# Performance work log

Hardware: AMD Instinct MI355X
Metric: run time of the kernel (lower is better)

The kernel has to match this reference:

```python
import jax, jax.numpy as jnp
import numpy as np

# graph sizes
G, P, EP = 128, 256, 1024          # graphs, nodes/graph, edges/graph
N, E = G * P, G * EP
C, KENS, S = 4, 2, 1               # centroids, ensembles, samples
R = S * KENS                       # repeats
F, DE, D, OUT = 64, 16, 128, 10


def setup_inputs() -> dict:
    key = jax.random.key(0)
    ks = jax.random.split(key, 24)
    off = (jnp.arange(G, dtype=jnp.int32) * P)[:, None]
    src = (jax.random.randint(ks[0], (G, EP), 0, P, dtype=jnp.int32) + off).reshape(-1)
    dst = (jax.random.randint(ks[1], (G, EP), 0, P, dtype=jnp.int32) + off).reshape(-1)
    edge_index = jnp.stack([src, dst])            # [2, E], edges stay within graphs
    batch = jnp.repeat(jnp.arange(G, dtype=jnp.int32), P)  # [N]
    rn = lambda k, shp, s: jax.random.normal(k, shp, jnp.float32) * s
    return {
        "x_feat": rn(ks[2], (N, F), 1.0),
        "edge_attr": rn(ks[3], (E, DE), 1.0),
        "W_atom": rn(ks[4], (F, D), 0.1), "b_atom": jnp.zeros((D,), jnp.float32),
        "W_score": rn(ks[5], (D, C * KENS), 0.1),
        "W_edge": rn(ks[6], (DE, D), 0.1),
        "W_b2c": rn(ks[7], (D, D), 0.1),
        "W_bb": rn(ks[8], (D, D), 0.1), "W_bc": rn(ks[9], (D, D), 0.1),
        "W_cb": rn(ks[10], (D, D), 0.1), "W_cc": rn(ks[11], (D, D), 0.1),
        "W_sb": rn(ks[12], (D, D), 0.1), "W_sc": rn(ks[13], (D, D), 0.1),
        "W_inter": rn(ks[14], (D, D), 0.1), "b_inter": jnp.zeros((D,), jnp.float32),
        "W_out": rn(ks[15], (D, OUT), 0.1), "b_out": jnp.zeros((OUT,), jnp.float32),
        "edge_index": edge_index, "batch": batch,
    }


def reference(x_feat, edge_attr, W_atom, b_atom, W_score, W_edge, W_b2c,
              W_bb, W_bc, W_cb, W_cc, W_sb, W_sc, W_inter, b_inter,
              W_out, b_out, edge_index, batch):
    src, dst = edge_index[0], edge_index[1]
    # atom encoder + scorer + softmax sampler (marginals)
    x = x_feat @ W_atom + b_atom                                  # [N,D]
    scores = (x @ W_score).reshape(N, C, KENS)
    marg = jax.nn.softmax(scores, axis=1)                         # over centroids
    nm = jnp.broadcast_to(marg[None], (S, N, C, KENS))            # [S,N,C,KENS]
    nm = jnp.transpose(nm, (0, 3, 2, 1)).reshape(R, C, N)         # [R,C,N]
    em = nm[:, :, src] * nm[:, :, dst]                            # edge_mask [R,C,E]
    # base2centroid: masked MP on base graph + weighted segment-mean pooling
    edge_emb = edge_attr @ W_edge                                 # [E,D]
    h = jax.nn.relu(x @ W_b2c)                                    # [N,D]
    m = h[src] + edge_emb                                         # [E,D]
    agg = jnp.zeros((R, C, N, D), m.dtype).at[:, :, dst].add(em[..., None] * m)
    hm = h[None, None] + agg                                      # [R,C,N,D]
    denom = jnp.zeros((R, C, G), nm.dtype).at[:, :, batch].add(nm)
    num = jnp.zeros((R, C, G, D), hm.dtype).at[:, :, batch].add(nm[..., None] * hm)
    cent_x = jnp.transpose(num / (denom[..., None] + 1e-6), (0, 2, 1, 3))  # [R,G,C,D]
    # intra centroid-pair edge weights: triu pairs + diag, scatter over graphs
    iu, ju = np.triu_indices(C, 1)
    pi = np.concatenate([iu, np.arange(C)])
    pj = np.concatenate([ju, np.arange(C)])
    e2g = batch[src]
    w = jnp.zeros((R, pi.size, G), nm.dtype).at[:, :, e2g].add(
        nm[:, pi][:, :, src] * nm[:, pj][:, :, dst])              # [R,10,G]
    w = w.at[:, -C:, :].multiply(0.5)                             # halve diagonal counts
    wt = jnp.transpose(w, (0, 2, 1))                              # [R,G,10]
    Wcc = jnp.zeros((R, G, C, C), nm.dtype)
    Wcc = Wcc.at[:, :, pi, pj].add(wt).at[:, :, pj, pi].add(wt)   # to_undirected
    dg = jnp.arange(C)
    Wcc = Wcc.at[:, :, dg, dg].multiply(0.5)                      # self loops counted once
    Wcc = Wcc / (jax.lax.stop_gradient(jnp.max(Wcc)) + 1e-9)      # detached-max norm
    # hetero GNN layer: base->base, base->centroid, centroid->centroid, centroid->base
    agg_bb = jnp.zeros((N, D), x.dtype).at[dst].add(x[src] + edge_emb)           # [N,D]
    agg_bc = jnp.transpose(
        jnp.zeros((R, C, G, D), x.dtype).at[:, :, batch].add(nm[..., None] * x[None, None]),
        (0, 2, 1, 3))                                             # [R,G,C,D]
    agg_cc = jnp.einsum('rgij,rgjd->rgid', Wcc, cent_x)
    h_cent = jax.nn.relu(agg_bc @ W_bc + agg_cc @ W_cc + cent_x @ W_sc)          # [R,G,C,D]
    agg_cb = jnp.einsum('rcn,rncd->rnd', nm, h_cent[:, batch])                   # [R,N,D]
    h_base = jax.nn.relu(agg_bb[None] @ W_bb + agg_cb @ W_cb + x[None] @ W_sb)   # [R,N,D]
    # inter-ensemble mean pool, inter head, intra mean graph pool, intra head
    node_emb = jnp.mean(h_base, axis=0) @ W_inter + b_inter                      # [N,D]
    graph_emb = jnp.zeros((G, D), node_emb.dtype).at[batch].add(node_emb) / P    # [G,D]
    return graph_emb @ W_out + b_out                                             # [G,OUT]
```

## Files before the change

kernel.cpp:

```cpp
#include <hip/hip_runtime.h>
#include <hip/hip_bf16.h>

#define Nn 32768
#define Ee 131072
#define Gg 128
#define Dd 128
#define ASTR 1032

using bf16 = __hip_bfloat16;
typedef __attribute__((ext_vector_type(8))) short bf16x8;
typedef __attribute__((ext_vector_type(4))) float f32x4;

__device__ __forceinline__ float b2f(bf16 v){ return __bfloat162float(v); }
__device__ __forceinline__ bf16  f2b(float v){ return __float2bfloat16(v); }
__device__ __forceinline__ unsigned short bf16bits(float v){
  union { bf16 b; unsigned short u; } cv; cv.b = f2b(v); return cv.u;
}
__device__ __forceinline__ unsigned int packxh(float xv, float hv){
  return ((unsigned int)bf16bits(hv) << 16) | (unsigned int)bf16bits(xv);
}
__device__ __forceinline__ float upk_x(unsigned int v){ return __uint_as_float(v << 16); }
__device__ __forceinline__ float upk_h(unsigned int v){ return __uint_as_float(v & 0xffff0000u); }

__global__ __launch_bounds__(128)
void k_wrep(const float* __restrict__ Wbb, const float* __restrict__ Wsb,
            const float* __restrict__ Wcb, unsigned short* __restrict__ Wbbp,
            unsigned short* __restrict__ Wsbp, unsigned short* __restrict__ Wcbp) {
  int mat = blockIdx.x >> 7, n = blockIdx.x & 127, k = threadIdx.x;
  const float* src = (mat == 0) ? Wbb : (mat == 1) ? Wsb : Wcb;
  unsigned short* dst = (mat == 0) ? Wbbp : (mat == 1) ? Wsbp : Wcbp;
  dst[n*128 + k] = bf16bits(src[k*128 + n]);
}

__global__ __launch_bounds__(256)
void k_atom(const float* __restrict__ xf, const float* __restrict__ Wa,
            const float* __restrict__ ba, const float* __restrict__ Wsc,
            const float* __restrict__ Wb2c,
            unsigned int* __restrict__ xh, float* __restrict__ nmt) {
  __shared__ float sxf[32*64];
  __shared__ float sx[32*128];
  __shared__ float ss[32*8];
  __shared__ float sWsc[1024];
  int tid = threadIdx.x, n0 = blockIdx.x * 32;
  int ct = tid & 31, rt = tid >> 5;
  int c0 = ct*4, r0 = rt*4;
  for (int j = tid; j < 2048; j += 256) sxf[j] = xf[n0*64 + j];
  for (int j = tid; j < 1024; j += 256) sWsc[j] = Wsc[j];
  __syncthreads();
  float acc[4][4];
  #pragma unroll
  for (int i = 0; i < 4; ++i)
    #pragma unroll
    for (int j = 0; j < 4; ++j) acc[i][j] = ba[c0+j];
  for (int k = 0; k < 64; ++k) {
    float4 bv = *reinterpret_cast<const float4*>(&Wa[k*128 + c0]);
    #pragma unroll
    for (int i = 0; i < 4; ++i) {
      float a = sxf[(r0+i)*64 + k];
      acc[i][0] += a*bv.x; acc[i][1] += a*bv.y; acc[i][2] += a*bv.z; acc[i][3] += a*bv.w;
    }
  }
  #pragma unroll
  for (int i = 0; i < 4; ++i)
    #pragma unroll
    for (int j = 0; j < 4; ++j) sx[(r0+i)*128 + c0+j] = acc[i][j];
  __syncthreads();
  {
    int node = tid >> 3, col = tid & 7;
    float s = 0.f;
    for (int d = 0; d < 128; ++d) s += sx[node*128 + d] * sWsc[d*8 + col];
    ss[node*8 + col] = s;
  }
  __syncthreads();
  if (tid < 64) {
    int node = tid >> 1, k = tid & 1;
    float v0 = ss[node*8 + 0 + k], v1 = ss[node*8 + 2 + k];
    float v2 = ss[node*8 + 4 + k], v3 = ss[node*8 + 6 + k];
    float mx = fmaxf(fmaxf(v0, v1), fmaxf(v2, v3));
    float e0 = expf(v0-mx), e1 = expf(v1-mx), e2 = expf(v2-mx), e3 = expf(v3-mx);
    float inv = 1.f / (e0+e1+e2+e3);
    size_t nb = (size_t)(n0 + node)*8 + k*4;
    nmt[nb+0] = e0*inv; nmt[nb+1] = e1*inv; nmt[nb+2] = e2*inv; nmt[nb+3] = e3*inv;
  }
  float acc2[4][4];
  #pragma unroll
  for (int i = 0; i < 4; ++i)
    #pragma unroll
    for (int j = 0; j < 4; ++j) acc2[i][j] = 0.f;
  for (int k = 0; k < 128; ++k) {
    float4 bv = *reinterpret_cast<const float4*>(&Wb2c[k*128 + c0]);
    #pragma unroll
    for (int i = 0; i < 4; ++i) {
      float a = sx[(r0+i)*128 + k];
      acc2[i][0] += a*bv.x; acc2[i][1] += a*bv.y; acc2[i][2] += a*bv.z; acc2[i][3] += a*bv.w;
    }
  }
  #pragma unroll
  for (int i = 0; i < 4; ++i)
    #pragma unroll
    for (int j = 0; j < 4; ++j)
      xh[(size_t)(n0+r0+i)*128 + c0+j] = packxh(acc[i][j], fmaxf(acc2[i][j], 0.f));
}

__global__ __launch_bounds__(256)
void k_csr(const int* __restrict__ ei, const float* __restrict__ nmt,
           const float* __restrict__ ea,
           int* __restrict__ osrc, int* __restrict__ rowstart,
           float* __restrict__ sea, float* __restrict__ den) {
  __shared__ int cnt[256], off[256], sdl[1024], sorder[1024];
  __shared__ float sden[256*8];
  int t = threadIdx.x, g = blockIdx.x;
  cnt[t] = 0;
  __syncthreads();
  #pragma unroll
  for (int j = 0; j < 4; ++j) {
    int e = t + j*256;
    int dl = ei[Ee + g*1024 + e] - g*256;
    sdl[e] = dl;
    atomicAdd(&cnt[dl], 1);
  }
  {
    const float4* p = reinterpret_cast<const float4*>(nmt + (size_t)(g*256 + t)*8);
    float4 a = p[0], b = p[1];
    sden[t*8+0]=a.x; sden[t*8+1]=a.y; sden[t*8+2]=a.z; sden[t*8+3]=a.w;
    sden[t*8+4]=b.x; sden[t*8+5]=b.y; sden[t*8+6]=b.z; sden[t*8+7]=b.w;
  }
  __syncthreads();
  off[t] = cnt[t];
  __syncthreads();
  for (int s = 1; s < 256; s <<= 1) {
    int v = (t >= s) ? off[t - s] : 0;
    __syncthreads();
    off[t] += v;
    __syncthreads();
  }
  int startv = off[t] - cnt[t];
  int mycnt = cnt[t];
  rowstart[g*256 + t] = startv;
  off[t] = startv;
  __syncthreads();
  #pragma unroll
  for (int j = 0; j < 4; ++j) {
    int e = t + j*256;
    int pos = atomicAdd(&off[sdl[e]], 1);
    sorder[pos] = e;
    osrc[g*1024 + pos] = ei[g*1024 + e];
  }
  __syncthreads();
  float s0x=0,s0y=0,s0z=0,s0w=0, s1x=0,s1y=0,s1z=0,s1w=0;
  float s2x=0,s2y=0,s2z=0,s2w=0, s3x=0,s3y=0,s3z=0,s3w=0;
  for (int jj = startv; jj < startv + mycnt; ++jj) {
    int e = sorder[jj];
    const float4* er = reinterpret_cast<const float4*>(ea + ((size_t)g*1024 + e)*16);
    float4 a0 = er[0], a1 = er[1], a2 = er[2], a3 = er[3];
    s0x+=a0.x; s0y+=a0.y; s0z+=a0.z; s0w+=a0.w;
    s1x+=a1.x; s1y+=a1.y; s1z+=a1.z; s1w+=a1.w;
    s2x+=a2.x; s2y+=a2.y; s2z+=a2.z; s2w+=a2.w;
    s3x+=a3.x; s3y+=a3.y; s3z+=a3.z; s3w+=a3.w;
  }
  float4* so = reinterpret_cast<float4*>(sea + (size_t)(g*256 + t)*16);
  so[0] = make_float4(s0x,s0y,s0z,s0w);
  so[1] = make_float4(s1x,s1y,s1z,s1w);
  so[2] = make_float4(s2x,s2y,s2z,s2w);
  so[3] = make_float4(s3x,s3y,s3z,s3w);
  if (t < 8) {
    float s = 0.f;
    for (int p = 0; p < 256; ++p) s += sden[p*8 + t];
    den[t*Gg + g] = s;
  }
}

__global__ __launch_bounds__(256)
void k_edgesc(const int* __restrict__ ei, const float* __restrict__ nmt,
              const float* __restrict__ ea, float* __restrict__ wcc,
              unsigned int* __restrict__ maxbits, float* __restrict__ bnm,
              float* __restrict__ gea) {
  __shared__ float salpha[8*ASTR];
  __shared__ float sbeta[8*256];
  __shared__ float red[20];
  __shared__ float geap[4*128];
  int t = threadIdx.x, g = blockIdx.x;
  for (int j = t; j < 2048; j += 256) sbeta[j] = 0.f;
  if (t < 20) red[t] = 0.f;
  __syncthreads();
  float w[20];
  #pragma unroll
  for (int i = 0; i < 20; ++i) w[i] = 0.f;
  #pragma unroll
  for (int j = 0; j < 4; ++j) {
    int e = t + j*256;
    int s = ei[g*1024 + e], dd = ei[Ee + g*1024 + e];
    const float4* ps4 = reinterpret_cast<const float4*>(nmt + (size_t)s*8);
    const float4* pt4 = reinterpret_cast<const float4*>(nmt + (size_t)dd*8);
    float4 sv0 = ps4[0], sv1 = ps4[1], tv0 = pt4[0], tv1 = pt4[1];
    float ps[8] = {sv0.x,sv0.y,sv0.z,sv0.w,sv1.x,sv1.y,sv1.z,sv1.w};
    float pt[8] = {tv0.x,tv0.y,tv0.z,tv0.w,tv1.x,tv1.y,tv1.z,tv1.w};
    #pragma unroll
    for (int r = 0; r < 2; ++r) {
      int b = r*4;
      w[r*10+0] += ps[b+0]*pt[b+1]; w[r*10+1] += ps[b+0]*pt[b+2]; w[r*10+2] += ps[b+0]*pt[b+3];
      w[r*10+3] += ps[b+1]*pt[b+2]; w[r*10+4] += ps[b+1]*pt[b+3]; w[r*10+5] += ps[b+2]*pt[b+3];
      w[r*10+6] += ps[b+0]*pt[b+0]; w[r*10+7] += ps[b+1]*pt[b+1];
      w[r*10+8] += ps[b+2]*pt[b+2]; w[r*10+9] += ps[b+3]*pt[b+3];
    }
    int sl = s - g*256;
    #pragma unroll
    for (int rc = 0; rc < 8; ++rc) {
      float al = ps[rc]*pt[rc]*pt[rc];
      salpha[rc*ASTR + e] = al;
      atomicAdd(&sbeta[rc*256 + sl], al);
    }
  }
  #pragma unroll
  for (int i = 0; i < 20; ++i) {
    for (int off2 = 32; off2 > 0; off2 >>= 1) w[i] += __shfl_down(w[i], off2);
  }
  if ((t & 63) == 0) {
    #pragma unroll
    for (int i = 0; i < 20; ++i) atomicAdd(&red[i], w[i]);
  }
  __syncthreads();
  if (t < 32) {
    int r = t >> 4, ij = t & 15, i = ij >> 2, j = ij & 3;
    float v;
    if (i == j) v = 0.5f * red[r*10 + 6 + i];
    else { int a = i < j ? i : j, b = i < j ? j : i;
           int p = (a == 0) ? (b - 1) : (a == 1) ? (b + 1) : 5;
           v = red[r*10 + p]; }
    wcc[(r*Gg + g)*16 + ij] = v;
    atomicMax(maxbits, __float_as_uint(v));
  }
  int wv = t >> 6, l = t & 63;
  int j16 = l & 15, rb = l >> 4;
  float acc0 = 0.f, acc1 = 0.f;
  int ebase = wv*256;
  for (int ee = 0; ee < 256; ++ee) {
    float eav = ea[((size_t)g*1024 + ebase + ee)*16 + j16];
    acc0 += salpha[rb*ASTR + ebase + ee] * eav;
    acc1 += salpha[(rb+4)*ASTR + ebase + ee] * eav;
  }
  geap[wv*128 + l]      = acc0;
  geap[wv*128 + 64 + l] = acc1;
  __syncthreads();
  if (t < 128) {
    float s = geap[t] + geap[128+t] + geap[256+t] + geap[384+t];
    int rc = t >> 4, j = t & 15;
    gea[((size_t)rc*Gg + g)*16 + j] = s;
  }
  {
    float b0 = sbeta[0*256+t], b1 = sbeta[1*256+t], b2 = sbeta[2*256+t], b3 = sbeta[3*256+t];
    float b4 = sbeta[4*256+t], b5 = sbeta[5*256+t], b6 = sbeta[6*256+t], b7 = sbeta[7*256+t];
    float4* bo = reinterpret_cast<float4*>(bnm + (size_t)(g*256 + t)*8);
    bo[0] = make_float4(b0,b1,b2,b3);
    bo[1] = make_float4(b4,b5,b6,b7);
  }
}

__global__ __launch_bounds__(256)
void k_gather(const unsigned int* __restrict__ xh, const float* __restrict__ nmt,
              const float* __restrict__ bnm, const float* __restrict__ sea,
              const float* __restrict__ We, const int* __restrict__ osrc,
              const int* __restrict__ rowstart,
              unsigned short* __restrict__ aggbb16, float* __restrict__ pnum,
              float* __restrict__ pabc) {
  __shared__ float combN[8*128], combA[8*128];
  int t = threadIdx.x, d = t & 127, q = t >> 7;
  int g = blockIdx.x >> 4, e16 = blockIdx.x & 15;
  int nbase = g*256 + e16*16;
  float w[16];
  #pragma unroll
  for (int j = 0; j < 16; ++j) w[j] = We[j*128 + d];
  float aH[8] = {0,0,0,0,0,0,0,0};
  float aX[8] = {0,0,0,0,0,0,0,0};
  for (int nn = q; nn < 16; nn += 2) {
    int n = nbase + nn;
    unsigned int vn = xh[(size_t)n*128 + d];
    float xn = upk_x(vn), hn = upk_h(vn);
    const float4* pp = reinterpret_cast<const float4*>(nmt + (size_t)n*8);
    float4 p0 = pp[0], p1 = pp[1];
    float pc[8] = {p0.x,p0.y,p0.z,p0.w,p1.x,p1.y,p1.z,p1.w};
    const float4* bp = reinterpret_cast<const float4*>(bnm + (size_t)n*8);
    float4 b0 = bp[0], b1 = bp[1];
    float bt[8] = {b0.x,b0.y,b0.z,b0.w,b1.x,b1.y,b1.z,b1.w};
    #pragma unroll
    for (int rc = 0; rc < 8; ++rc) {
      aH[rc] += (pc[rc] + bt[rc])*hn;
      aX[rc] += pc[rc]*xn;
    }
    const float4* sp = reinterpret_cast<const float4*>(sea + (size_t)n*16);
    float4 s0 = sp[0], s1 = sp[1], s2 = sp[2], s3 = sp[3];
    float agg = s0.x*w[0] + s0.y*w[1] + s0.z*w[2] + s0.w*w[3]
              + s1.x*w[4] + s1.y*w[5] + s1.z*w[6] + s1.w*w[7]
              + s2.x*w[8] + s2.y*w[9] + s2.z*w[10]+ s2.w*w[11]
              + s3.x*w[12]+ s3.y*w[13]+ s3.z*w[14]+ s3.w*w[15];
    int ln = n - g*256;
    int start = rowstart[n];
    int end = (ln == 255) ? 1024 : rowstart[n+1];
    for (int jj = start; jj < end; ++jj) {
      int sg = osrc[g*1024 + jj];
      agg += upk_x(xh[(size_t)sg*128 + d]);
    }
    aggbb16[(size_t)n*128 + d] = bf16bits(agg);
  }
  if (q == 1) {
    #pragma unroll
    for (int rc = 0; rc < 8; ++rc) { combN[rc*128+d] = aH[rc]; combA[rc*128+d] = aX[rc]; }
  }
  __syncthreads();
  if (q == 0) {
    #pragma unroll
    for (int rc = 0; rc < 8; ++rc) {
      pnum[(((size_t)rc*Gg + g)*16 + e16)*128 + d] = aH[rc] + combN[rc*128+d];
      pabc[(((size_t)rc*Gg + g)*16 + e16)*128 + d] = aX[rc] + combA[rc*128+d];
    }
  }
}

__global__ __launch_bounds__(128)
void k_hcent(const float* __restrict__ pnum, const float* __restrict__ den,
             const float* __restrict__ pabc, const float* __restrict__ gea,
             const float* __restrict__ We, const float* __restrict__ wcc,
             const unsigned int* __restrict__ maxbits,
             const float* __restrict__ Wbc, const float* __restrict__ Wcc_,
             const float* __restrict__ Wsc2, float* __restrict__ hcent) {
  __shared__ float scent[512], sbc[512], sccs[512], swcc[16];
  int tid = threadIdx.x, r = blockIdx.x >> 7, g = blockIdx.x & 127;
  float inv = 1.f / (__uint_as_float(*maxbits) + 1e-9f);
  if (tid < 16) swcc[tid] = wcc[(r*Gg + g)*16 + tid] * inv;
  for (int c = 0; c < 4; ++c) {
    int rc = r*4 + c;
    float nv = 0.f, av = 0.f;
    #pragma unroll
    for (int s = 0; s < 16; ++s) {
      nv += pnum[(((size_t)rc*Gg + g)*16 + s)*128 + tid];
      av += pabc[(((size_t)rc*Gg + g)*16 + s)*128 + tid];
    }
    const float* geag = gea + ((size_t)rc*Gg + g)*16;
    #pragma unroll
    for (int j = 0; j < 16; ++j) nv += geag[j] * We[j*128 + tid];
    float dn = den[rc*Gg + g] + 1e-6f;
    scent[c*128 + tid] = nv / dn;
    sbc[c*128 + tid]   = av;
  }
  __syncthreads();
  for (int i = 0; i < 4; ++i) {
    sccs[i*128 + tid] = swcc[i*4+0]*scent[tid]       + swcc[i*4+1]*scent[128 + tid]
                      + swcc[i*4+2]*scent[256 + tid] + swcc[i*4+3]*scent[384 + tid];
  }
  __syncthreads();
  float acc[4] = {0.f, 0.f, 0.f, 0.f};
  for (int k = 0; k < 128; ++k) {
    float wb = Wbc[k*128 + tid], wc = Wcc_[k*128 + tid], ws2 = Wsc2[k*128 + tid];
    #pragma unroll
    for (int c = 0; c < 4; ++c)
      acc[c] += sbc[c*128 + k]*wb + sccs[c*128 + k]*wc + scent[c*128 + k]*ws2;
  }
  #pragma unroll
  for (int c = 0; c < 4; ++c)
    hcent[((r*Gg + g)*4 + c)*128 + tid] = fmaxf(acc[c], 0.f);
}

__global__ __launch_bounds__(256)
void k_hbase(const unsigned short* __restrict__ aggbb16,
             const unsigned int* __restrict__ xh,
             const float* __restrict__ nmt, const float* __restrict__ hcent,
             const unsigned short* __restrict__ Wbbp,
             const unsigned short* __restrict__ Wsbp,
             const unsigned short* __restrict__ Wcbp,
             float* __restrict__ gsum) {
  __shared__ unsigned short A1[64*136];
  __shared__ unsigned short A2[64*136];
  __shared__ float shc[512];
  __shared__ float snm[256];
  __shared__ float pred[128];
  int tid = threadIdx.x, n0 = blockIdx.x*64, g = n0 >> 8;
  int lane = tid & 63, wv = tid >> 6;
  int m = lane & 15, quad = lane >> 4;
  int rbase = wv*16;
  for (int j = tid; j < 1024; j += 256) {
    int row = j >> 4, col = (j & 15) * 8;
    uint4 v = *reinterpret_cast<const uint4*>(aggbb16 + (size_t)(n0+row)*128 + col);
    *reinterpret_cast<uint4*>(&A1[row*136 + col]) = v;
  }
  for (int j = tid; j < 2048; j += 256) {
    int row = j >> 5, col = (j & 31) * 4;
    uint4 v = *reinterpret_cast<const uint4*>(xh + (size_t)(n0+row)*128 + col);
    uint2 o;
    o.x = (v.x & 0xffffu) | (v.y << 16);
    o.y = (v.z & 0xffffu) | (v.w << 16);
    *reinterpret_cast<uint2*>(&A2[row*136 + col]) = o;
  }
  __syncthreads();
  f32x4 bb[8];
  #pragma unroll
  for (int nt = 0; nt < 8; ++nt) bb[nt] = (f32x4){0.f,0.f,0.f,0.f};
  const short* a1r = (const short*)&A1[(rbase + m)*136];
  const short* a2r = (const short*)&A2[(rbase + m)*136];
  #pragma unroll
  for (int nt = 0; nt < 8; ++nt) {
    #pragma unroll
    for (int kk = 0; kk < 4; ++kk) {
      int ko = kk*32 + quad*8;
      bf16x8 av1 = *reinterpret_cast<const bf16x8*>(a1r + ko);
      bf16x8 wv1 = *reinterpret_cast<const bf16x8*>((const short*)Wbbp + (nt*16 + m)*128 + ko);
      bb[nt] = __builtin_amdgcn_mfma_f32_16x16x32_bf16(av1, wv1, bb[nt], 0, 0, 0);
      bf16x8 av2 = *reinterpret_cast<const bf16x8*>(a2r + ko);
      bf16x8 wv2 = *reinterpret_cast<const bf16x8*>((const short*)Wsbp + (nt*16 + m)*128 + ko);
      bb[nt] = __builtin_amdgcn_mfma_f32_16x16x32_bf16(av2, wv2, bb[nt], 0, 0, 0);
    }
  }
  __syncthreads();
  unsigned short* SB = A2;
  f32x4 msum[8];
  #pragma unroll
  for (int nt = 0; nt < 8; ++nt) msum[nt] = (f32x4){0.f,0.f,0.f,0.f};
  for (int r = 0; r < 2; ++r) {
    for (int j = tid; j < 512; j += 256) shc[j] = hcent[((size_t)(r*Gg + g)*4)*128 + j];
    if (tid < 256) snm[tid] = nmt[(size_t)(n0 + (tid >> 2))*8 + r*4 + (tid & 3)];
    __syncthreads();
    for (int j = tid; j < 8192; j += 256) {
      int node = j >> 7, k = j & 127;
      float v = snm[node*4+0]*shc[k]       + snm[node*4+1]*shc[128 + k]
              + snm[node*4+2]*shc[256 + k] + snm[node*4+3]*shc[384 + k];
      SB[node*136 + k] = bf16bits(v);
    }
    __syncthreads();
    f32x4 aw[8];
    #pragma unroll
    for (int nt = 0; nt < 8; ++nt) aw[nt] = (f32x4){0.f,0.f,0.f,0.f};
    const short* sbr = (const short*)&SB[(rbase + m)*136];
    #pragma unroll
    for (int nt = 0; nt < 8; ++nt) {
      #pragma unroll
      for (int kk = 0; kk < 4; ++kk) {
        int ko = kk*32 + quad*8;
        bf16x8 av = *reinterpret_cast<const bf16x8*>(sbr + ko);
        bf16x8 wvv = *reinterpret_cast<const bf16x8*>((const short*)Wcbp + (nt*16 + m)*128 + ko);
        aw[nt] = __builtin_amdgcn_mfma_f32_16x16x32_bf16(av, wvv, aw[nt], 0, 0, 0);
      }
    }
    #pragma unroll
    for (int nt = 0; nt < 8; ++nt) {
      #pragma unroll
      for (int i = 0; i < 4; ++i)
        msum[nt][i] += 0.5f * fmaxf(bb[nt][i] + aw[nt][i], 0.f);
    }
    __syncthreads();
  }
  if (tid < 128) pred[tid] = 0.f;
  __syncthreads();
  #pragma unroll
  for (int nt = 0; nt < 8; ++nt) {
    float s = msum[nt][0] + msum[nt][1] + msum[nt][2] + msum[nt][3];
    atomicAdd(&pred[nt*16 + m], s);
  }
  __syncthreads();
  if (tid < 128) atomicAdd(&gsum[g*128 + tid], pred[tid]);
}

__global__ __launch_bounds__(128)
void k_out(const float* __restrict__ gsum, const float* __restrict__ Wint,
           const float* __restrict__ bint, const float* __restrict__ Wout,
           const float* __restrict__ bout, float* __restrict__ out) {
  __shared__ float ss[128], sge[128];
  int tid = threadIdx.x, g = blockIdx.x;
  ss[tid] = gsum[g*128 + tid] * (1.f/256.f);
  __syncthreads();
  float ge = bint[tid];
  for (int k = 0; k < 128; ++k) ge += ss[k] * Wint[k*128 + tid];
  sge[tid] = ge;
  __syncthreads();
  if (tid < 10) {
    float o = bout[tid];
    for (int d = 0; d < 128; ++d) o += sge[d] * Wout[d*10 + tid];
    out[g*10 + tid] = o;
  }
}

extern "C" void kernel_launch(void* const* d_in, const int* in_sizes, int n_in,
                              void* d_out, int out_size, void* d_ws, size_t ws_size,
                              hipStream_t stream) {
  const float* xf   = (const float*)d_in[0];
  const float* ea   = (const float*)d_in[1];
  const float* Wa   = (const float*)d_in[2];
  const float* ba   = (const float*)d_in[3];
  const float* Wsc  = (const float*)d_in[4];
  const float* We   = (const float*)d_in[5];
  const float* Wb2c = (const float*)d_in[6];
  const float* Wbb  = (const float*)d_in[7];
  const float* Wbc  = (const float*)d_in[8];
  const float* Wcb  = (const float*)d_in[9];
  const float* WccW = (const float*)d_in[10];
  const float* Wsb  = (const float*)d_in[11];
  const float* Wsc2 = (const float*)d_in[12];
  const float* Wint = (const float*)d_in[13];
  const float* bint = (const float*)d_in[14];
  const float* Wout = (const float*)d_in[15];
  const float* bout = (const float*)d_in[16];
  const int*   ei   = (const int*)d_in[17];

  float* ws    = (float*)d_ws;
  unsigned int* xh = (unsigned int*)ws;
  float* nmt   = ws + 4194304;
  float* hcent = ws + 4456448;
  float* wcc   = ws + 4587520;
  unsigned short* aggbb16 = (unsigned short*)(ws + 4591616);
  int*   osrc  = (int*)(ws + 6688768);
  int*   rowst = (int*)(ws + 6819840);
  float* sea   = ws + 6852608;
  float* bnm   = ws + 7376896;
  float* gea   = ws + 7639040;
  float* pnum  = ws + 7655424;
  float* pabc  = ws + 9752576;
  float* den   = ws + 11849728;
  float* gsum  = ws + 11850752;
  unsigned int* maxbits = (unsigned int*)(ws + 11867136);
  unsigned short* Wbbp = (unsigned short*)(ws + 11867200);
  unsigned short* Wsbp = (unsigned short*)(ws + 11875392);
  unsigned short* Wcbp = (unsigned short*)(ws + 11883584);

  hipMemsetAsync(gsum, 0, (16384 + 64) * sizeof(float), stream);

  k_wrep  <<<3*128, 128, 0, stream>>>(Wbb, Wsb, Wcb, Wbbp, Wsbp, Wcbp);
  k_atom  <<<Nn/32, 256, 0, stream>>>(xf, Wa, ba, Wsc, Wb2c, xh, nmt);
  k_csr   <<<Gg,    256, 0, stream>>>(ei, nmt, ea, osrc, rowst, sea, den);
  k_edgesc<<<Gg,    256, 0, stream>>>(ei, nmt, ea, wcc, maxbits, bnm, gea);
  k_gather<<<Gg*16, 256, 0, stream>>>(xh, nmt, bnm, sea, We, osrc, rowst,
                                      aggbb16, pnum, pabc);
  k_hcent <<<2*Gg,  128, 0, stream>>>(pnum, den, pabc, gea, We, wcc, maxbits,
                                      Wbc, WccW, Wsc2, hcent);
  k_hbase <<<Nn/64, 256, 0, stream>>>(aggbb16, xh, nmt, hcent, Wbbp, Wsbp, Wcbp, gsum);
  k_out   <<<Gg,    128, 0, stream>>>(gsum, Wint, bint, Wout, bout, (float*)d_out);
}
```

Baseline: 293.3 us.

## Use MFMA for atom encoder, fuse CSR and edge-score kernels, split gather

The atom encoder and b2c projection move from scalar fp32 FMA loops to bf16 MFMA 16x16x32, with transposed bf16 copies of W_atom and W_b2c prepared in the weight-repack kernel. The CSR build and the edge-scoring kernel are merged into one per-graph kernel that stages edge attributes in LDS chunks and accumulates per-node edge-attr sums with shared atomics. The old gather kernel is split into a pooling kernel and an edge-aggregation kernel with finer granularity, giving more blocks. The aim is to cut scalar compute and kernel-launch and global-read overhead. The cost is bf16 rounding of the x activations before the score and b2c products, plus heavier LDS atomic traffic.

```diff
diff --git a/kernel.cpp b/kernel.cpp
--- a/kernel.cpp
+++ b/kernel.cpp
@@ -5,7 +5,6 @@
 #define Ee 131072
 #define Gg 128
 #define Dd 128
-#define ASTR 1032
 
 using bf16 = __hip_bfloat16;
 typedef __attribute__((ext_vector_type(8))) short bf16x8;
@@ -16,114 +15,160 @@
 __device__ __forceinline__ unsigned short bf16bits(float v){
   union { bf16 b; unsigned short u; } cv; cv.b = f2b(v); return cv.u;
 }
-__device__ __forceinline__ unsigned int packxh(float xv, float hv){
-  return ((unsigned int)bf16bits(hv) << 16) | (unsigned int)bf16bits(xv);
+__device__ __forceinline__ float bfu(unsigned short u){
+  return __uint_as_float((unsigned int)u << 16);
 }
 __device__ __forceinline__ float upk_x(unsigned int v){ return __uint_as_float(v << 16); }
 __device__ __forceinline__ float upk_h(unsigned int v){ return __uint_as_float(v & 0xffff0000u); }
 
 __global__ __launch_bounds__(128)
 void k_wrep(const float* __restrict__ Wbb, const float* __restrict__ Wsb,
-            const float* __restrict__ Wcb, unsigned short* __restrict__ Wbbp,
-            unsigned short* __restrict__ Wsbp, unsigned short* __restrict__ Wcbp) {
+            const float* __restrict__ Wcb, const float* __restrict__ Wa,
+            const float* __restrict__ Wb2c,
+            unsigned short* __restrict__ Wbbp, unsigned short* __restrict__ Wsbp,
+            unsigned short* __restrict__ Wcbp, unsigned short* __restrict__ Wap,
+            unsigned short* __restrict__ Wb2cp) {
   int mat = blockIdx.x >> 7, n = blockIdx.x & 127, k = threadIdx.x;
-  const float* src = (mat == 0) ? Wbb : (mat == 1) ? Wsb : Wcb;
-  unsigned short* dst = (mat == 0) ? Wbbp : (mat == 1) ? Wsbp : Wcbp;
-  dst[n*128 + k] = bf16bits(src[k*128 + n]);
+  if      (mat == 0) Wbbp [n*128 + k] = bf16bits(Wbb [k*128 + n]);
+  else if (mat == 1) Wsbp [n*128 + k] = bf16bits(Wsb [k*128 + n]);
+  else if (mat == 2) Wcbp [n*128 + k] = bf16bits(Wcb [k*128 + n]);
+  else if (mat == 3) { if (k < 64) Wap[n*64 + k] = bf16bits(Wa[k*128 + n]); }
+  else               Wb2cp[n*128 + k] = bf16bits(Wb2c[k*128 + n]);
 }
 
 __global__ __launch_bounds__(256)
-void k_atom(const float* __restrict__ xf, const float* __restrict__ Wa,
+void k_atom(const float* __restrict__ xf, const unsigned short* __restrict__ Wap,
             const float* __restrict__ ba, const float* __restrict__ Wsc,
-            const float* __restrict__ Wb2c,
+            const unsigned short* __restrict__ Wb2cp,
             unsigned int* __restrict__ xh, float* __restrict__ nmt) {
-  __shared__ float sxf[32*64];
-  __shared__ float sx[32*128];
-  __shared__ float ss[32*8];
+  __shared__ unsigned short sxf[64*72];
+  __shared__ unsigned short sxb[64*136];
+  __shared__ float ss[64*8];
   __shared__ float sWsc[1024];
-  int tid = threadIdx.x, n0 = blockIdx.x * 32;
-  int ct = tid & 31, rt = tid >> 5;
-  int c0 = ct*4, r0 = rt*4;
-  for (int j = tid; j < 2048; j += 256) sxf[j] = xf[n0*64 + j];
+  int tid = threadIdx.x, n0 = blockIdx.x*64;
+  int lane = tid & 63, wv = tid >> 6;
+  int m = lane & 15, quad = lane >> 4;
+  int rbase = wv*16;
+  #pragma unroll
+  for (int k = 0; k < 4; ++k) {
+    int pos = (tid + k*256)*4;
+    int node = pos >> 6, f = pos & 63;
+    float4 v = *reinterpret_cast<const float4*>(xf + (size_t)n0*64 + pos);
+    ushort4 o;
+    o.x = bf16bits(v.x); o.y = bf16bits(v.y); o.z = bf16bits(v.z); o.w = bf16bits(v.w);
+    *reinterpret_cast<ushort4*>(&sxf[node*72 + f]) = o;
+  }
   for (int j = tid; j < 1024; j += 256) sWsc[j] = Wsc[j];
   __syncthreads();
-  float acc[4][4];
-  #pragma unroll
-  for (int i = 0; i < 4; ++i)
-    #pragma unroll
-    for (int j = 0; j < 4; ++j) acc[i][j] = ba[c0+j];
-  for (int k = 0; k < 64; ++k) {
-    float4 bv = *reinterpret_cast<const float4*>(&Wa[k*128 + c0]);
-    #pragma unroll
-    for (int i = 0; i < 4; ++i) {
-      float a = sxf[(r0+i)*64 + k];
-      acc[i][0] += a*bv.x; acc[i][1] += a*bv.y; acc[i][2] += a*bv.z; acc[i][3] += a*bv.w;
-    }
-  }
-  #pragma unroll
-  for (int i = 0; i < 4; ++i)
-    #pragma unroll
-    for (int j = 0; j < 4; ++j) sx[(r0+i)*128 + c0+j] = acc[i][j];
-  __syncthreads();
-  {
-    int node = tid >> 3, col = tid & 7;
+  f32x4 cx[8];
+  #pragma unroll
+  for (int nt = 0; nt < 8; ++nt) {
+    float bv = ba[nt*16 + m];
+    cx[nt] = (f32x4){bv, bv, bv, bv};
+  }
+  const unsigned short* a1 = &sxf[(rbase + m)*72];
+  #pragma unroll
+  for (int nt = 0; nt < 8; ++nt) {
+    #pragma unroll
+    for (int kk = 0; kk < 2; ++kk) {
+      int ko = kk*32 + quad*8;
+      bf16x8 av = *reinterpret_cast<const bf16x8*>((const short*)a1 + ko);
+      bf16x8 bv8 = *reinterpret_cast<const bf16x8*>((const short*)Wap + (nt*16 + m)*64 + ko);
+      cx[nt] = __builtin_amdgcn_mfma_f32_16x16x32_bf16(av, bv8, cx[nt], 0, 0, 0);
+    }
+  }
+  #pragma unroll
+  for (int nt = 0; nt < 8; ++nt)
+    #pragma unroll
+    for (int i = 0; i < 4; ++i)
+      sxb[(rbase + quad*4 + i)*136 + nt*16 + m] = bf16bits(cx[nt][i]);
+  __syncthreads();
+  for (int p = tid; p < 512; p += 256) {
+    int node = p >> 3, col = p & 7;
     float s = 0.f;
-    for (int d = 0; d < 128; ++d) s += sx[node*128 + d] * sWsc[d*8 + col];
+    for (int dd = 0; dd < 128; ++dd)
+      s += bfu(sxb[node*136 + dd]) * sWsc[dd*8 + col];
     ss[node*8 + col] = s;
   }
   __syncthreads();
-  if (tid < 64) {
+  if (tid < 128) {
     int node = tid >> 1, k = tid & 1;
     float v0 = ss[node*8 + 0 + k], v1 = ss[node*8 + 2 + k];
     float v2 = ss[node*8 + 4 + k], v3 = ss[node*8 + 6 + k];
     float mx = fmaxf(fmaxf(v0, v1), fmaxf(v2, v3));
     float e0 = expf(v0-mx), e1 = expf(v1-mx), e2 = expf(v2-mx), e3 = expf(v3-mx);
     float inv = 1.f / (e0+e1+e2+e3);
-    size_t nb = (size_t)(n0 + node)*8 + k*4;
-    nmt[nb+0] = e0*inv; nmt[nb+1] = e1*inv; nmt[nb+2] = e2*inv; nmt[nb+3] = e3*inv;
-  }
-  float acc2[4][4];
-  #pragma unroll
-  for (int i = 0; i < 4; ++i)
-    #pragma unroll
-    for (int j = 0; j < 4; ++j) acc2[i][j] = 0.f;
-  for (int k = 0; k < 128; ++k) {
-    float4 bv = *reinterpret_cast<const float4*>(&Wb2c[k*128 + c0]);
+    *reinterpret_cast<float4*>(nmt + (size_t)(n0 + node)*8 + k*4) =
+        make_float4(e0*inv, e1*inv, e2*inv, e3*inv);
+  }
+  f32x4 chf[8];
+  #pragma unroll
+  for (int nt = 0; nt < 8; ++nt) chf[nt] = (f32x4){0.f,0.f,0.f,0.f};
+  const unsigned short* a2 = &sxb[(rbase + m)*136];
+  #pragma unroll
+  for (int nt = 0; nt < 8; ++nt) {
+    #pragma unroll
+    for (int kk = 0; kk < 4; ++kk) {
+      int ko = kk*32 + quad*8;
+      bf16x8 av = *reinterpret_cast<const bf16x8*>((const short*)a2 + ko);
+      bf16x8 bv8 = *reinterpret_cast<const bf16x8*>((const short*)Wb2cp + (nt*16 + m)*128 + ko);
+      chf[nt] = __builtin_amdgcn_mfma_f32_16x16x32_bf16(av, bv8, chf[nt], 0, 0, 0);
+    }
+  }
+  #pragma unroll
+  for (int nt = 0; nt < 8; ++nt) {
     #pragma unroll
     for (int i = 0; i < 4; ++i) {
-      float a = sx[(r0+i)*128 + k];
-      acc2[i][0] += a*bv.x; acc2[i][1] += a*bv.y; acc2[i][2] += a*bv.z; acc2[i][3] += a*bv.w;
-    }
-  }
-  #pragma unroll
-  for (int i = 0; i < 4; ++i)
-    #pragma unroll
-    for (int j = 0; j < 4; ++j)
-      xh[(size_t)(n0+r0+i)*128 + c0+j] = packxh(acc[i][j], fmaxf(acc2[i][j], 0.f));
+      int row = rbase + quad*4 + i, col = nt*16 + m;
+      float hv = fmaxf(chf[nt][i], 0.f);
+      unsigned short xb = sxb[row*136 + col];
+      xh[(size_t)(n0 + row)*128 + col] =
+          ((unsigned int)bf16bits(hv) << 16) | (unsigned int)xb;
+    }
+  }
 }
 
 __global__ __launch_bounds__(256)
-void k_csr(const int* __restrict__ ei, const float* __restrict__ nmt,
-           const float* __restrict__ ea,
-           int* __restrict__ osrc, int* __restrict__ rowstart,
-           float* __restrict__ sea, float* __restrict__ den) {
-  __shared__ int cnt[256], off[256], sdl[1024], sorder[1024];
-  __shared__ float sden[256*8];
+void k_graph(const int* __restrict__ ei, const float* __restrict__ nmt,
+             const float* __restrict__ ea,
+             int* __restrict__ osrc, int* __restrict__ rowstart,
+             float* __restrict__ sea, float* __restrict__ den,
+             float* __restrict__ wcc, unsigned int* __restrict__ maxbits,
+             float* __restrict__ bnm, float* __restrict__ gea) {
+  __shared__ int sdl[1024], ssl[1024];
+  __shared__ int cnt[256], off[256];
+  __shared__ float eabuf[256*16];
+  __shared__ float salpha[8*258];
+  __shared__ float sbeta[8*256];
+  __shared__ float seaacc[256*17];
+  __shared__ float red[20];
+  __shared__ float sga[256];
+  __shared__ float den8[8];
   int t = threadIdx.x, g = blockIdx.x;
   cnt[t] = 0;
+  for (int j = t; j < 2048; j += 256) sbeta[j] = 0.f;
+  for (int j = t; j < 4352; j += 256) seaacc[j] = 0.f;
+  if (t < 20) red[t] = 0.f;
+  if (t < 8) den8[t] = 0.f;
   __syncthreads();
   #pragma unroll
   for (int j = 0; j < 4; ++j) {
     int e = t + j*256;
+    int sl = ei[g*1024 + e] - g*256;
     int dl = ei[Ee + g*1024 + e] - g*256;
-    sdl[e] = dl;
+    ssl[e] = sl; sdl[e] = dl;
     atomicAdd(&cnt[dl], 1);
   }
   {
     const float4* p = reinterpret_cast<const float4*>(nmt + (size_t)(g*256 + t)*8);
     float4 a = p[0], b = p[1];
-    sden[t*8+0]=a.x; sden[t*8+1]=a.y; sden[t*8+2]=a.z; sden[t*8+3]=a.w;
-    sden[t*8+4]=b.x; sden[t*8+5]=b.y; sden[t*8+6]=b.z; sden[t*8+7]=b.w;
+    float v[8] = {a.x,a.y,a.z,a.w,b.x,b.y,b.z,b.w};
+    #pragma unroll
+    for (int i = 0; i < 8; ++i) {
+      float s = v[i];
+      for (int o = 32; o > 0; o >>= 1) s += __shfl_xor(s, o);
+      if ((t & 63) == 0) atomicAdd(&den8[i], s);
+    }
   }
   __syncthreads();
   off[t] = cnt[t];
@@ -135,7 +180,6 @@
     __syncthreads();
   }
   int startv = off[t] - cnt[t];
-  int mycnt = cnt[t];
   rowstart[g*256 + t] = startv;
   off[t] = startv;
   __syncthreads();
@@ -143,82 +187,67 @@
   for (int j = 0; j < 4; ++j) {
     int e = t + j*256;
     int pos = atomicAdd(&off[sdl[e]], 1);
-    sorder[pos] = e;
-    osrc[g*1024 + pos] = ei[g*1024 + e];
-  }
-  __syncthreads();
-  float s0x=0,s0y=0,s0z=0,s0w=0, s1x=0,s1y=0,s1z=0,s1w=0;
-  float s2x=0,s2y=0,s2z=0,s2w=0, s3x=0,s3y=0,s3z=0,s3w=0;
-  for (int jj = startv; jj < startv + mycnt; ++jj) {
-    int e = sorder[jj];
-    const float4* er = reinterpret_cast<const float4*>(ea + ((size_t)g*1024 + e)*16);
-    float4 a0 = er[0], a1 = er[1], a2 = er[2], a3 = er[3];
-    s0x+=a0.x; s0y+=a0.y; s0z+=a0.z; s0w+=a0.w;
-    s1x+=a1.x; s1y+=a1.y; s1z+=a1.z; s1w+=a1.w;
-    s2x+=a2.x; s2y+=a2.y; s2z+=a2.z; s2w+=a2.w;
-    s3x+=a3.x; s3y+=a3.y; s3z+=a3.z; s3w+=a3.w;
-  }
-  float4* so = reinterpret_cast<float4*>(sea + (size_t)(g*256 + t)*16);
-  so[0] = make_float4(s0x,s0y,s0z,s0w);
-  so[1] = make_float4(s1x,s1y,s1z,s1w);
-  so[2] = make_float4(s2x,s2y,s2z,s2w);
-  so[3] = make_float4(s3x,s3y,s3z,s3w);
-  if (t < 8) {
-    float s = 0.f;
-    for (int p = 0; p < 256; ++p) s += sden[p*8 + t];
-    den[t*Gg + g] = s;
-  }
-}
-
-__global__ __launch_bounds__(256)
-void k_edgesc(const int* __restrict__ ei, const float* __restrict__ nmt,
-              const float* __restrict__ ea, float* __restrict__ wcc,
-              unsigned int* __restrict__ maxbits, float* __restrict__ bnm,
-              float* __restrict__ gea) {
-  __shared__ float salpha[8*ASTR];
-  __shared__ float sbeta[8*256];
-  __shared__ float red[20];
-  __shared__ float geap[4*128];
-  int t = threadIdx.x, g = blockIdx.x;
-  for (int j = t; j < 2048; j += 256) sbeta[j] = 0.f;
-  if (t < 20) red[t] = 0.f;
-  __syncthreads();
-  float w[20];
-  #pragma unroll
-  for (int i = 0; i < 20; ++i) w[i] = 0.f;
-  #pragma unroll
-  for (int j = 0; j < 4; ++j) {
-    int e = t + j*256;
-    int s = ei[g*1024 + e], dd = ei[Ee + g*1024 + e];
-    const float4* ps4 = reinterpret_cast<const float4*>(nmt + (size_t)s*8);
-    const float4* pt4 = reinterpret_cast<const float4*>(nmt + (size_t)dd*8);
-    float4 sv0 = ps4[0], sv1 = ps4[1], tv0 = pt4[0], tv1 = pt4[1];
-    float ps[8] = {sv0.x,sv0.y,sv0.z,sv0.w,sv1.x,sv1.y,sv1.z,sv1.w};
-    float pt[8] = {tv0.x,tv0.y,tv0.z,tv0.w,tv1.x,tv1.y,tv1.z,tv1.w};
-    #pragma unroll
-    for (int r = 0; r < 2; ++r) {
-      int b = r*4;
-      w[r*10+0] += ps[b+0]*pt[b+1]; w[r*10+1] += ps[b+0]*pt[b+2]; w[r*10+2] += ps[b+0]*pt[b+3];
-      w[r*10+3] += ps[b+1]*pt[b+2]; w[r*10+4] += ps[b+1]*pt[b+3]; w[r*10+5] += ps[b+2]*pt[b+3];
-      w[r*10+6] += ps[b+0]*pt[b+0]; w[r*10+7] += ps[b+1]*pt[b+1];
-      w[r*10+8] += ps[b+2]*pt[b+2]; w[r*10+9] += ps[b+3]*pt[b+3];
-    }
-    int sl = s - g*256;
-    #pragma unroll
-    for (int rc = 0; rc < 8; ++rc) {
-      float al = ps[rc]*pt[rc]*pt[rc];
-      salpha[rc*ASTR + e] = al;
-      atomicAdd(&sbeta[rc*256 + sl], al);
+    osrc[g*1024 + pos] = g*256 + ssl[e];
+  }
+  float w20[20];
+  #pragma unroll
+  for (int i = 0; i < 20; ++i) w20[i] = 0.f;
+  float greg = 0.f;
+  int grc = t >> 5, gj = (t >> 1) & 15, ghf = t & 1;
+  for (int ch = 0; ch < 4; ++ch) {
+    __syncthreads();
+    for (int j = t; j < 1024; j += 256)
+      reinterpret_cast<float4*>(eabuf)[j] =
+        reinterpret_cast<const float4*>(ea + (size_t)(g*1024 + ch*256)*16)[j];
+    {
+      int e = ch*256 + t;
+      int sl = ssl[e], dl = sdl[e];
+      const float4* ps4 = reinterpret_cast<const float4*>(nmt + (size_t)(g*256 + sl)*8);
+      const float4* pt4 = reinterpret_cast<const float4*>(nmt + (size_t)(g*256 + dl)*8);
+      float4 sv0 = ps4[0], sv1 = ps4[1], tv0 = pt4[0], tv1 = pt4[1];
+      float ps[8] = {sv0.x,sv0.y,sv0.z,sv0.w,sv1.x,sv1.y,sv1.z,sv1.w};
+      float pt[8] = {tv0.x,tv0.y,tv0.z,tv0.w,tv1.x,tv1.y,tv1.z,tv1.w};
+      #pragma unroll
+      for (int r = 0; r < 2; ++r) {
+        int b = r*4;
+        w20[r*10+0] += ps[b+0]*pt[b+1]; w20[r*10+1] += ps[b+0]*pt[b+2];
+        w20[r*10+2] += ps[b+0]*pt[b+3]; w20[r*10+3] += ps[b+1]*pt[b+2];
+        w20[r*10+4] += ps[b+1]*pt[b+3]; w20[r*10+5] += ps[b+2]*pt[b+3];
+        w20[r*10+6] += ps[b+0]*pt[b+0]; w20[r*10+7] += ps[b+1]*pt[b+1];
+        w20[r*10+8] += ps[b+2]*pt[b+2]; w20[r*10+9] += ps[b+3]*pt[b+3];
+      }
+      #pragma unroll
+      for (int rc = 0; rc < 8; ++rc) {
+        float al = ps[rc]*pt[rc]*pt[rc];
+        salpha[rc*258 + t] = al;
+        atomicAdd(&sbeta[rc*256 + sl], al);
+      }
+    }
+    __syncthreads();
+    {
+      int e = ch*256 + t;
+      int dl = sdl[e];
+      #pragma unroll
+      for (int j2 = 0; j2 < 16; ++j2)
+        atomicAdd(&seaacc[dl*17 + j2], eabuf[t*16 + j2]);
+    }
+    {
+      float a = 0.f;
+      int eb = ghf*128;
+      for (int ee = eb; ee < eb + 128; ++ee)
+        a += salpha[grc*258 + ee] * eabuf[ee*16 + gj];
+      greg += a;
     }
   }
   #pragma unroll
   for (int i = 0; i < 20; ++i) {
-    for (int off2 = 32; off2 > 0; off2 >>= 1) w[i] += __shfl_down(w[i], off2);
+    for (int o = 32; o > 0; o >>= 1) w20[i] += __shfl_down(w20[i], o);
   }
   if ((t & 63) == 0) {
     #pragma unroll
-    for (int i = 0; i < 20; ++i) atomicAdd(&red[i], w[i]);
-  }
+    for (int i = 0; i < 20; ++i) atomicAdd(&red[i], w20[i]);
+  }
+  sga[t] = greg;
   __syncthreads();
   if (t < 32) {
     int r = t >> 4, ij = t & 15, i = ij >> 2, j = ij & 3;
@@ -230,46 +259,33 @@
     wcc[(r*Gg + g)*16 + ij] = v;
     atomicMax(maxbits, __float_as_uint(v));
   }
-  int wv = t >> 6, l = t & 63;
-  int j16 = l & 15, rb = l >> 4;
-  float acc0 = 0.f, acc1 = 0.f;
-  int ebase = wv*256;
-  for (int ee = 0; ee < 256; ++ee) {
-    float eav = ea[((size_t)g*1024 + ebase + ee)*16 + j16];
-    acc0 += salpha[rb*ASTR + ebase + ee] * eav;
-    acc1 += salpha[(rb+4)*ASTR + ebase + ee] * eav;
-  }
-  geap[wv*128 + l]      = acc0;
-  geap[wv*128 + 64 + l] = acc1;
-  __syncthreads();
-  if (t < 128) {
-    float s = geap[t] + geap[128+t] + geap[256+t] + geap[384+t];
-    int rc = t >> 4, j = t & 15;
-    gea[((size_t)rc*Gg + g)*16 + j] = s;
+  if ((t & 1) == 0) {
+    float s = sga[t] + sga[t+1];
+    gea[((size_t)grc*Gg + g)*16 + gj] = s;
   }
   {
-    float b0 = sbeta[0*256+t], b1 = sbeta[1*256+t], b2 = sbeta[2*256+t], b3 = sbeta[3*256+t];
-    float b4 = sbeta[4*256+t], b5 = sbeta[5*256+t], b6 = sbeta[6*256+t], b7 = sbeta[7*256+t];
     float4* bo = reinterpret_cast<float4*>(bnm + (size_t)(g*256 + t)*8);
-    bo[0] = make_float4(b0,b1,b2,b3);
-    bo[1] = make_float4(b4,b5,b6,b7);
-  }
+    bo[0] = make_float4(sbeta[0*256+t], sbeta[1*256+t], sbeta[2*256+t], sbeta[3*256+t]);
+    bo[1] = make_float4(sbeta[4*256+t], sbeta[5*256+t], sbeta[6*256+t], sbeta[7*256+t]);
+  }
+  {
+    float4* so = reinterpret_cast<float4*>(sea + (size_t)(g*256 + t)*16);
+    so[0] = make_float4(seaacc[t*17+0],  seaacc[t*17+1],  seaacc[t*17+2],  seaacc[t*17+3]);
+    so[1] = make_float4(seaacc[t*17+4],  seaacc[t*17+5],  seaacc[t*17+6],  seaacc[t*17+7]);
+    so[2] = make_float4(seaacc[t*17+8],  seaacc[t*17+9],  seaacc[t*17+10], seaacc[t*17+11]);
+    so[3] = make_float4(seaacc[t*17+12], seaacc[t*17+13], seaacc[t*17+14], seaacc[t*17+15]);
+  }
+  if (t < 8) den[t*Gg + g] = den8[t];
 }
 
 __global__ __launch_bounds__(256)
-void k_gather(const unsigned int* __restrict__ xh, const float* __restrict__ nmt,
-              const float* __restrict__ bnm, const float* __restrict__ sea,
-              const float* __restrict__ We, const int* __restrict__ osrc,
-              const int* __restrict__ rowstart,
-              unsigned short* __restrict__ aggbb16, float* __restrict__ pnum,
-              float* __restrict__ pabc) {
+void k_pool(const unsigned int* __restrict__ xh, const float* __restrict__ nmt,
+            const float* __restrict__ bnm, float* __restrict__ pnum,
+            float* __restrict__ pabc) {
   __shared__ float combN[8*128], combA[8*128];
   int t = threadIdx.x, d = t & 127, q = t >> 7;
   int g = blockIdx.x >> 4, e16 = blockIdx.x & 15;
   int nbase = g*256 + e16*16;
-  float w[16];
-  #pragma unroll
-  for (int j = 0; j < 16; ++j) w[j] = We[j*128 + d];
   float aH[8] = {0,0,0,0,0,0,0,0};
   float aX[8] = {0,0,0,0,0,0,0,0};
   for (int nn = q; nn < 16; nn += 2) {
@@ -287,13 +303,40 @@
       aH[rc] += (pc[rc] + bt[rc])*hn;
       aX[rc] += pc[rc]*xn;
     }
+  }
+  if (q == 1) {
+    #pragma unroll
+    for (int rc = 0; rc < 8; ++rc) { combN[rc*128+d] = aH[rc]; combA[rc*128+d] = aX[rc]; }
+  }
+  __syncthreads();
+  if (q == 0) {
+    #pragma unroll
+    for (int rc = 0; rc < 8; ++rc) {
+      pnum[(((size_t)rc*Gg + g)*16 + e16)*128 + d] = aH[rc] + combN[rc*128+d];
+      pabc[(((size_t)rc*Gg + g)*16 + e16)*128 + d] = aX[rc] + combA[rc*128+d];
+    }
+  }
+}
+
+__global__ __launch_bounds__(256)
+void k_aggx(const unsigned int* __restrict__ xh, const float* __restrict__ sea,
+            const float* __restrict__ We, const int* __restrict__ osrc,
+            const int* __restrict__ rowstart, unsigned short* __restrict__ aggbb16) {
+  int t = threadIdx.x, d = t & 127, q = t >> 7;
+  int g = blockIdx.x >> 5, e32 = blockIdx.x & 31;
+  int nbase = g*256 + e32*8;
+  float w[16];
+  #pragma unroll
+  for (int j = 0; j < 16; ++j) w[j] = We[j*128 + d];
+  for (int nn = q; nn < 8; nn += 2) {
+    int n = nbase + nn;
     const float4* sp = reinterpret_cast<const float4*>(sea + (size_t)n*16);
     float4 s0 = sp[0], s1 = sp[1], s2 = sp[2], s3 = sp[3];
     float agg = s0.x*w[0] + s0.y*w[1] + s0.z*w[2] + s0.w*w[3]
               + s1.x*w[4] + s1.y*w[5] + s1.z*w[6] + s1.w*w[7]
               + s2.x*w[8] + s2.y*w[9] + s2.z*w[10]+ s2.w*w[11]
               + s3.x*w[12]+ s3.y*w[13]+ s3.z*w[14]+ s3.w*w[15];
-    int ln = n - g*256;
+    int ln = n & 255;
     int start = rowstart[n];
     int end = (ln == 255) ? 1024 : rowstart[n+1];
     for (int jj = start; jj < end; ++jj) {
@@ -301,18 +344,6 @@
       agg += upk_x(xh[(size_t)sg*128 + d]);
     }
     aggbb16[(size_t)n*128 + d] = bf16bits(agg);
-  }
-  if (q == 1) {
-    #pragma unroll
-    for (int rc = 0; rc < 8; ++rc) { combN[rc*128+d] = aH[rc]; combA[rc*128+d] = aX[rc]; }
-  }
-  __syncthreads();
-  if (q == 0) {
-    #pragma unroll
-    for (int rc = 0; rc < 8; ++rc) {
-      pnum[(((size_t)rc*Gg + g)*16 + e16)*128 + d] = aH[rc] + combN[rc*128+d];
-      pabc[(((size_t)rc*Gg + g)*16 + e16)*128 + d] = aX[rc] + combA[rc*128+d];
-    }
   }
 }
 
@@ -515,20 +546,23 @@
   float* den   = ws + 11849728;
   float* gsum  = ws + 11850752;
   unsigned int* maxbits = (unsigned int*)(ws + 11867136);
-  unsigned short* Wbbp = (unsigned short*)(ws + 11867200);
-  unsigned short* Wsbp = (unsigned short*)(ws + 11875392);
-  unsigned short* Wcbp = (unsigned short*)(ws + 11883584);
+  unsigned short* Wbbp  = (unsigned short*)(ws + 11867200);
+  unsigned short* Wsbp  = (unsigned short*)(ws + 11875392);
+  unsigned short* Wcbp  = (unsigned short*)(ws + 11883584);
+  unsigned short* Wap   = (unsigned short*)(ws + 11891776);
+  unsigned short* Wb2cp = (unsigned short*)(ws + 11895872);
 
   hipMemsetAsync(gsum, 0, (16384 + 64) * sizeof(float), stream);
 
-  k_wrep  <<<3*128, 128, 0, stream>>>(Wbb, Wsb, Wcb, Wbbp, Wsbp, Wcbp);
-  k_atom  <<<Nn/32, 256, 0, stream>>>(xf, Wa, ba, Wsc, Wb2c, xh, nmt);
-  k_csr   <<<Gg,    256, 0, stream>>>(ei, nmt, ea, osrc, rowst, sea, den);
-  k_edgesc<<<Gg,    256, 0, stream>>>(ei, nmt, ea, wcc, maxbits, bnm, gea);
-  k_gather<<<Gg*16, 256, 0, stream>>>(xh, nmt, bnm, sea, We, osrc, rowst,
-                                      aggbb16, pnum, pabc);
-  k_hcent <<<2*Gg,  128, 0, stream>>>(pnum, den, pabc, gea, We, wcc, maxbits,
-                                      Wbc, WccW, Wsc2, hcent);
-  k_hbase <<<Nn/64, 256, 0, stream>>>(aggbb16, xh, nmt, hcent, Wbbp, Wsbp, Wcbp, gsum);
-  k_out   <<<Gg,    128, 0, stream>>>(gsum, Wint, bint, Wout, bout, (float*)d_out);
-}
+  k_wrep <<<5*128, 128, 0, stream>>>(Wbb, Wsb, Wcb, Wa, Wb2c,
+                                     Wbbp, Wsbp, Wcbp, Wap, Wb2cp);
+  k_atom <<<Nn/64, 256, 0, stream>>>(xf, Wap, ba, Wsc, Wb2cp, xh, nmt);
+  k_graph<<<Gg,    256, 0, stream>>>(ei, nmt, ea, osrc, rowst, sea, den,
+                                     wcc, maxbits, bnm, gea);
+  k_pool <<<Gg*16, 256, 0, stream>>>(xh, nmt, bnm, pnum, pabc);
+  k_aggx <<<Gg*32, 256, 0, stream>>>(xh, sea, We, osrc, rowst, aggbb16);
+  k_hcent<<<2*Gg,  128, 0, stream>>>(pnum, den, pabc, gea, We, wcc, maxbits,
+                                     Wbc, WccW, Wsc2, hcent);
+  k_hbase<<<Nn/64, 256, 0, stream>>>(aggbb16, xh, nmt, hcent, Wbbp, Wsbp, Wcbp, gsum);
+  k_out  <<<Gg,    128, 0, stream>>>(gsum, Wint, bint, Wout, bout, (float*)d_out);
+}
```

Measured after the change: 294.6 us. No clear change (+0.5%).
